# Optimization experiments

Measured on AMD Instinct MI355X. Metric: run time of the kernel, lower is better.

The kernel has to match this reference:

```python
import jax, jax.numpy as jnp
import numpy as np

N_NODES = 100000
N_EDGES = 1600000
IN_F = 16
HID = 128
N_LAYERS = 8
BN_EPS = 1e-5


def bn(x, gamma, beta):
    # BatchNorm1d in training mode: batch statistics over the node axis
    mu = jnp.mean(x, axis=0)
    var = jnp.var(x, axis=0)
    return gamma * (x - mu) * jax.lax.rsqrt(var + BN_EPS) + beta


def setup_inputs() -> dict:
    key = jax.random.key(0)
    ks = jax.random.split(key, 20)
    inp = {
        'x': jax.random.normal(ks[0], (N_NODES, IN_F), dtype=jnp.float32),
        'edge_index': jax.random.randint(ks[1], (2, N_EDGES), 0, N_NODES, dtype=jnp.int32),
        'eps': jnp.zeros((N_LAYERS,), jnp.float32),  # train_eps init 0
        # GIN MLPs: layer 0 has in_feature input, layers 1..7 have hidden input
        'W1_0': 0.1 * jax.random.normal(ks[2], (IN_F, HID), dtype=jnp.float32),
        'b1_0': jnp.zeros((HID,), jnp.float32),
        'W1': 0.1 * jax.random.normal(ks[3], (N_LAYERS - 1, HID, HID), dtype=jnp.float32),
        'b1': jnp.zeros((N_LAYERS - 1, HID), jnp.float32),
        'g_in': jnp.ones((N_LAYERS, HID), jnp.float32),   # inner MLP BatchNorm gamma
        'be_in': jnp.zeros((N_LAYERS, HID), jnp.float32),  # inner MLP BatchNorm beta
        'W2': 0.1 * jax.random.normal(ks[4], (N_LAYERS, HID, HID), dtype=jnp.float32),
        'b2': jnp.zeros((N_LAYERS, HID), jnp.float32),
        'g_out': jnp.ones((N_LAYERS, HID), jnp.float32),   # per-layer outer BatchNorm gamma
        'be_out': jnp.zeros((N_LAYERS, HID), jnp.float32),
        'Wr1': 0.1 * jax.random.normal(ks[5], (HID, HID), dtype=jnp.float32),
        'br1': jnp.zeros((HID,), jnp.float32),
        'gr': jnp.ones((HID,), jnp.float32),
        'ber': jnp.zeros((HID,), jnp.float32),
        'Wr2': 0.1 * jax.random.normal(ks[6], (HID, 1), dtype=jnp.float32),
        'br2': jnp.zeros((1,), jnp.float32),
    }
    return inp


def reference(x, edge_index, eps, W1_0, b1_0, W1, b1, g_in, be_in, W2, b2,
              g_out, be_out, Wr1, br1, gr, ber, Wr2, br2):
    src = edge_index[0]
    dst = edge_index[1]
    n = x.shape[0]
    h = x
    skip_sum = jnp.zeros((n, HID), x.dtype)
    for i in range(N_LAYERS):
        # GINConv: nn((1 + eps) * x + sum_{j in N(i)} x_j)
        agg = jax.ops.segment_sum(h[src], dst, num_segments=n)  # scatter-add over edges
        z = (1.0 + eps[i]) * h + agg
        Wa = W1_0 if i == 0 else W1[i - 1]
        ba = b1_0 if i == 0 else b1[i - 1]
        z = jax.nn.relu(bn(z @ Wa + ba, g_in[i], be_in[i]))  # MLP hidden layer (dropout=0)
        z = z @ W2[i] + b2[i]                                 # MLP output layer
        h = jax.nn.relu(bn(z, g_out[i], be_out[i]))           # outer BatchNorm + ReLU
        if i % 2 == 1:  # skips after layers 2, 4, 6, 8
            skip_sum = skip_sum + h
    h = skip_sum / 4.0
    r = jax.nn.relu(bn(h @ Wr1 + br1, gr, ber))
    return jax.nn.sigmoid(r @ Wr2 + br2)  # [N, 1]
```

## Files before the change

### kernel.cpp

```cpp
#include <hip/hip_runtime.h>
#include <hip/hip_bf16.h>

#define NNODES 100000
#define NEDGES 1600000
#define IN_F 16
#define HID 128
#define NLAYERS 8
#define BN_EPS 1e-5f
#define BLOBSZ 532480
#define NCLS 32

typedef __attribute__((ext_vector_type(8))) short short8;
typedef __attribute__((ext_vector_type(8))) _Float16 f16x8;
typedef __attribute__((ext_vector_type(4))) float f32x4;
typedef __attribute__((ext_vector_type(4))) unsigned int uint32x4;
typedef unsigned short ushort_t;
typedef unsigned int uint_t;

__device__ __forceinline__ float f16l(uint_t u) {
  return (float)__builtin_bit_cast(_Float16, (ushort_t)(u & 0xFFFFu));
}
__device__ __forceinline__ float f16h(uint_t u) {
  return (float)__builtin_bit_cast(_Float16, (ushort_t)(u >> 16));
}
// ... 20 lines not shown
__global__ __launch_bounds__(256) void bhist_kernel(
    const int* __restrict__ dst, int* __restrict__ bucketCnt, int E, int nbk) {
  __shared__ int cnt[256];
  int t = threadIdx.x;
  cnt[t] = 0;
  __syncthreads();
  int base = blockIdx.x * 2048 + t * 8;
#pragma unroll
  for (int j = 0; j < 8; ++j) {
    int i = base + j;
    if (i < E) atomicAdd(&cnt[dst[i] >> 9], 1);
  }
  __syncthreads();
  if (t < nbk && cnt[t]) atomicAdd(&bucketCnt[t], cnt[t]);
}

__global__ void bscan_kernel(const int* __restrict__ bucketCnt, int* __restrict__ bucketBase,
                             int* __restrict__ bucketCur, int* __restrict__ row_ptr,
                             int N, int E, int nbk) {
  __shared__ int s[256];
  int t = threadIdx.x;
  s[t] = (t < nbk) ? bucketCnt[t] : 0;
  __syncthreads();
  for (int off = 1; off < 256; off <<= 1) {
    int v = (t >= off) ? s[t - off] : 0;
    __syncthreads();
    s[t] += v;
    __syncthreads();
  }
  int excl = (t == 0) ? 0 : s[t - 1];
  if (t < nbk) { bucketBase[t] = excl; bucketCur[t] = excl; }
  if (t == nbk) bucketBase[t] = E;
  if (t == 0) row_ptr[N] = E;
}

__global__ __launch_bounds__(256) void bscatter_kernel(
    const int* __restrict__ src, const int* __restrict__ dst,
    int* __restrict__ bucketCur, int2* __restrict__ ebuf, int E, int nbk) {
  __shared__ int cnt[256];
  __shared__ int base_l[256];
  int t = threadIdx.x;
  cnt[t] = 0;
  __syncthreads();
  int base = blockIdx.x * 2048 + t * 8;
  int bj[8], lr[8], dj[8], sj[8];
#pragma unroll
  for (int j = 0; j < 8; ++j) {
    int i = base + j;
    if (i < E) {
      dj[j] = dst[i];
      sj[j] = src[i];
      bj[j] = dj[j] >> 9;
      lr[j] = atomicAdd(&cnt[bj[j]], 1);
    } else bj[j] = -1;
  }
  __syncthreads();
  if (t < nbk) base_l[t] = cnt[t] ? atomicAdd(&bucketCur[t], cnt[t]) : 0;
  __syncthreads();
#pragma unroll
  for (int j = 0; j < 8; ++j)
    if (bj[j] >= 0) ebuf[base_l[bj[j]] + lr[j]] = make_int2(dj[j], sj[j]);
}

__global__ __launch_bounds__(256) void bcsr_kernel(
    const int2* __restrict__ ebuf, const int* __restrict__ bucketBase,
    int* __restrict__ row_ptr, int* __restrict__ colb, int N) {
  __shared__ int h[512];
  __shared__ int cur[512];
  __shared__ int s2[256];
  int b = blockIdx.x, t = threadIdx.x;
  int beg = bucketBase[b], end = bucketBase[b + 1];
  h[t] = 0; h[t + 256] = 0;
  __syncthreads();
  for (int p = beg + t; p < end; p += 256) atomicAdd(&h[ebuf[p].x & 511], 1);
  __syncthreads();
  s2[t] = h[2 * t] + h[2 * t + 1];
  __syncthreads();
  for (int off = 1; off < 256; off <<= 1) {
    int v = (t >= off) ? s2[t - off] : 0;
    __syncthreads();
    s2[t] += v;
    __syncthreads();
  }
  int ep = (t == 0) ? 0 : s2[t - 1];
  cur[2 * t] = ep;
  cur[2 * t + 1] = ep + h[2 * t];
  int dg = (b << 9) + 2 * t;
  if (dg < N) row_ptr[dg] = beg + cur[2 * t];
  if (dg + 1 < N) row_ptr[dg + 1] = beg + cur[2 * t + 1];
  __syncthreads();
  for (int p = beg + t; p < end; p += 256) {
    int2 e2 = ebuf[p];
    int pos = beg + atomicAdd(&cur[e2.x & 511], 1);
    colb[pos] = e2.y;
  }
}

__global__ void preconv_kernel(const float* __restrict__ W1_0, const float* __restrict__ W1,
                               const float* __restrict__ W2, const float* __restrict__ Wr1,
                               ushort_t* __restrict__ WB) {
  int g = blockIdx.y;
  int e = blockIdx.x * 256 + threadIdx.x;
  int KP = (g == 0) ? 32 : 128;
  if (e >= KP * 128) return;
  int k = e >> 7, n = e & 127;
  float v;
  if (g == 0) v = (k < 16) ? W1_0[k * 128 + n] : 0.0f;
  else if (g <= 7) v = W1[(size_t)(g - 1) * 16384 + e];
  else if (g <= 15) v = W2[(size_t)(g - 8) * 16384 + e];
  else v = Wr1[e];
  size_t base = (g == 0) ? 0 : (8192 + (size_t)(g - 1) * 32768);
  int unit = ((k >> 5) << 9) + ((n >> 4) << 6) + (n & 15) + (((k >> 3) & 3) << 4);
  WB[base + (size_t)unit * 8 + (k & 7)] = __builtin_bit_cast(ushort_t, (_Float16)v);
}

__global__ __launch_bounds__(256) void agg16_kernel(
    const float* __restrict__ X, const int* __restrict__ rp, const int* __restrict__ colb,
    const float* __restrict__ eps, float* __restrict__ Z, int N) {
  int g = threadIdx.x >> 3;
  int l = threadIdx.x & 7;
  int n = blockIdx.x * 32 + g;
  if (n >= N) return;
  float e = 1.0f + eps[0];
  const float2* X2 = (const float2*)X;
  float2 self = X2[(size_t)n * 8 + l];
  float2 acc = make_float2(self.x * e, self.y * e);
  float2 acc2 = make_float2(0.0f, 0.0f);
  int beg = rp[n], end = rp[n + 1];
  int p = beg;
  for (; p + 4 <= end; p += 4) {
    int s0 = colb[p], s1 = colb[p + 1], s2 = colb[p + 2], s3 = colb[p + 3];
    float2 v0 = X2[(size_t)s0 * 8 + l];
    float2 v1 = X2[(size_t)s1 * 8 + l];
    float2 v2 = X2[(size_t)s2 * 8 + l];
    float2 v3 = X2[(size_t)s3 * 8 + l];
    acc.x += v0.x; acc.y += v0.y;
    acc2.x += v1.x; acc2.y += v1.y;
    acc.x += v2.x; acc.y += v2.y;
    acc2.x += v3.x; acc2.y += v3.y;
  }
  for (; p < end; ++p) {
    int s = colb[p];
    float2 v = X2[(size_t)s * 8 + l];
    acc.x += v.x; acc.y += v.y;
  }
  acc.x += acc2.x; acc.y += acc2.y;
  ((float2*)Z)[(size_t)n * 8 + l] = acc;
}

__global__ __launch_bounds__(256) void agg128_kernel(
    const ushort_t* __restrict__ Y, const float* __restrict__ av, const float* __restrict__ cv,
    const int* __restrict__ rp, const int* __restrict__ colb,
    const float* __restrict__ eps, int layer, uint_t* __restrict__ Z,
    float* __restrict__ SKIP, int smode, int N) {
  int wv = threadIdx.x >> 6;
  int lane = threadIdx.x & 63;
  int half = lane >> 5;
  int l32 = lane & 31;
  int n = blockIdx.x * 4 + wv;
  if (n >= N) return;
  float e = 1.0f + eps[layer];
  float4 a4 = *(const float4*)(av + l32 * 4);
  float4 c4 = *(const float4*)(cv + l32 * 4);
  const uint2* Y2 = (const uint2*)Y;
  uint2 sv = Y2[(size_t)n * 32 + l32];
  float h0 = fmaxf(fmaf(a4.x, f16l(sv.x), c4.x), 0.0f);
  float h1 = fmaxf(fmaf(a4.y, f16h(sv.x), c4.y), 0.0f);
  float h2 = fmaxf(fmaf(a4.z, f16l(sv.y), c4.z), 0.0f);
  float h3 = fmaxf(fmaf(a4.w, f16h(sv.y), c4.w), 0.0f);
  if (half == 0) {
    if (smode == 1) {
      ((float4*)SKIP)[(size_t)n * 32 + l32] = make_float4(h0, h1, h2, h3);
    } else if (smode == 2) {
      float4* S4 = (float4*)SKIP;
      float4 s = S4[(size_t)n * 32 + l32];
      s.x += h0; s.y += h1; s.z += h2; s.w += h3;
      S4[(size_t)n * 32 + l32] = s;
    }
  }
  float ax0 = half ? 0.0f : h0 * e;
  float ax1 = half ? 0.0f : h1 * e;
  float ax2 = half ? 0.0f : h2 * e;
  float ax3 = half ? 0.0f : h3 * e;
  float bx0 = 0.0f, bx1 = 0.0f, bx2 = 0.0f, bx3 = 0.0f;
  int beg = rp[n], end = rp[n + 1];
  int p = beg;
  for (; p + 8 <= end; p += 8) {
    int s0 = colb[p + half];
    int s1 = colb[p + 2 + half];
    int s2 = colb[p + 4 + half];
    int s3 = colb[p + 6 + half];
    uint2 v0 = Y2[(size_t)s0 * 32 + l32];
    uint2 v1 = Y2[(size_t)s1 * 32 + l32];
    uint2 v2 = Y2[(size_t)s2 * 32 + l32];
    uint2 v3 = Y2[(size_t)s3 * 32 + l32];
    ax0 += fmaxf(fmaf(a4.x, f16l(v0.x), c4.x), 0.0f);
    ax1 += fmaxf(fmaf(a4.y, f16h(v0.x), c4.y), 0.0f);
    ax2 += fmaxf(fmaf(a4.z, f16l(v0.y), c4.z), 0.0f);
    ax3 += fmaxf(fmaf(a4.w, f16h(v0.y), c4.w), 0.0f);
    bx0 += fmaxf(fmaf(a4.x, f16l(v1.x), c4.x), 0.0f);
    bx1 += fmaxf(fmaf(a4.y, f16h(v1.x), c4.y), 0.0f);
    bx2 += fmaxf(fmaf(a4.z, f16l(v1.y), c4.z), 0.0f);
    bx3 += fmaxf(fmaf(a4.w, f16h(v1.y), c4.w), 0.0f);
    ax0 += fmaxf(fmaf(a4.x, f16l(v2.x), c4.x), 0.0f);
    ax1 += fmaxf(fmaf(a4.y, f16h(v2.x), c4.y), 0.0f);
    ax2 += fmaxf(fmaf(a4.z, f16l(v2.y), c4.z), 0.0f);
    ax3 += fmaxf(fmaf(a4.w, f16h(v2.y), c4.w), 0.0f);
    bx0 += fmaxf(fmaf(a4.x, f16l(v3.x), c4.x), 0.0f);
    bx1 += fmaxf(fmaf(a4.y, f16h(v3.x), c4.y), 0.0f);
    bx2 += fmaxf(fmaf(a4.z, f16l(v3.y), c4.z), 0.0f);
    bx3 += fmaxf(fmaf(a4.w, f16h(v3.y), c4.w), 0.0f);
  }
  for (; p + 2 <= end; p += 2) {
    int s = colb[p + half];
    uint2 v = Y2[(size_t)s * 32 + l32];
    ax0 += fmaxf(fmaf(a4.x, f16l(v.x), c4.x), 0.0f);
    ax1 += fmaxf(fmaf(a4.y, f16h(v.x), c4.y), 0.0f);
    ax2 += fmaxf(fmaf(a4.z, f16l(v.y), c4.z), 0.0f);
    ax3 += fmaxf(fmaf(a4.w, f16h(v.y), c4.w), 0.0f);
  }
  if (p < end && half == 0) {
    int s = colb[p];
    uint2 v = Y2[(size_t)s * 32 + l32];
    ax0 += fmaxf(fmaf(a4.x, f16l(v.x), c4.x), 0.0f);
    ax1 += fmaxf(fmaf(a4.y, f16h(v.x), c4.y), 0.0f);
    ax2 += fmaxf(fmaf(a4.z, f16l(v.y), c4.z), 0.0f);
    ax3 += fmaxf(fmaf(a4.w, f16h(v.y), c4.w), 0.0f);
  }
  ax0 += bx0; ax1 += bx1; ax2 += bx2; ax3 += bx3;
  ax0 += __shfl_xor(ax0, 32, 64);
  ax1 += __shfl_xor(ax1, 32, 64);
  ax2 += __shfl_xor(ax2, 32, 64);
  ax3 += __shfl_xor(ax3, 32, 64);
  if (half == 0) {
    uint2 o;
    o.x = pk16(ax0, ax1);
    o.y = pk16(ax2, ax3);
    ((uint2*)Z)[(size_t)n * 32 + l32] = o;
  }
}

template <int KTOT, int MODE, int OUT>
__global__ __launch_bounds__(256, 4) void gemm_mfma(
    const float* __restrict__ A, const ushort_t* __restrict__ A2u,
    const ushort_t* __restrict__ Bhi,
    const float* __restrict__ bias,
    const float* __restrict__ pa, const float* __restrict__ pc,
    void* __restrict__ Cv,
    float* __restrict__ gstat,
    float* __restrict__ aout, float* __restrict__ cout, int* __restrict__ cnt,
    const float* __restrict__ gamma, const float* __restrict__ beta,
    float invN, int M, int nb) {
  __shared__ float s_part[4][256];
  __shared__ int s_last;
  const int tid = threadIdx.x;
  const int w = tid >> 6;
  const int lane = tid & 63;
  const int ln = lane & 15;
  const int quad = lane >> 4;
  const int brow = blockIdx.x * 128;
  constexpr int AST = (MODE == 3) ? 16 : 128;

  int r0 = brow + (w << 5) + ln;       if (r0 >= M) r0 = M - 1;
  int r1 = brow + (w << 5) + 16 + ln;  if (r1 >= M) r1 = M - 1;

  f32x4 acc[2][8];
#pragma unroll
  for (int rt = 0; rt < 2; ++rt)
#pragma unroll
    for (int ct = 0; ct < 8; ++ct) acc[rt][ct] = (f32x4){0.0f, 0.0f, 0.0f, 0.0f};

  constexpr int KC = KTOT / 32;
#pragma unroll
  for (int kcl = 0; kcl < KC; ++kcl) {
    const int kb = (kcl << 5) + (quad << 3);
    f16x8 af0, af1;
    if constexpr (MODE == 0) {
      af0 = __builtin_bit_cast(f16x8, ntl_s8(A2u + (size_t)r0 * 128 + kb));
      af1 = __builtin_bit_cast(f16x8, ntl_s8(A2u + (size_t)r1 * 128 + kb));
    } else if constexpr (MODE == 1) {
      uint32x4 xa = *(const uint32x4*)(A2u + (size_t)r0 * 128 + kb);
      uint32x4 xb = *(const uint32x4*)(A2u + (size_t)r1 * 128 + kb);
      float4 p0 = *(const float4*)(pa + kb);
      float4 p1 = *(const float4*)(pa + kb + 4);
      float4 q0 = *(const float4*)(pc + kb);
      float4 q1 = *(const float4*)(pc + kb + 4);
      float pp[8] = {p0.x, p0.y, p0.z, p0.w, p1.x, p1.y, p1.z, p1.w};
      float qq[8] = {q0.x, q0.y, q0.z, q0.w, q1.x, q1.y, q1.z, q1.w};
      float e0[8] = {f16l(xa.x), f16h(xa.x), f16l(xa.y), f16h(xa.y),
                     f16l(xa.z), f16h(xa.z), f16l(xa.w), f16h(xa.w)};
      float e1[8] = {f16l(xb.x), f16h(xb.x), f16l(xb.y), f16h(xb.y),
                     f16l(xb.z), f16h(xb.z), f16l(xb.w), f16h(xb.w)};
#pragma unroll
      for (int j = 0; j < 8; ++j) {
        e0[j] = fmaxf(fmaf(pp[j], e0[j], qq[j]), 0.0f);
        e1[j] = fmaxf(fmaf(pp[j], e1[j], qq[j]), 0.0f);
      }
      af0 = pack8(e0);
      af1 = pack8(e1);
    } else if constexpr (MODE == 2) {
      f32x4 a0 = ntl4(A + (size_t)r0 * AST + kb);
      f32x4 a1 = ntl4(A + (size_t)r0 * AST + kb + 4);
      f32x4 b0 = ntl4(A + (size_t)r1 * AST + kb);
      f32x4 b1 = ntl4(A + (size_t)r1 * AST + kb + 4);
      float s0[8] = {a0.x, a0.y, a0.z, a0.w, a1.x, a1.y, a1.z, a1.w};
      float s1[8] = {b0.x, b0.y, b0.z, b0.w, b1.x, b1.y, b1.z, b1.w};
      uint32x4 ya = *(const uint32x4*)(A2u + (size_t)r0 * 128 + kb);
      uint32x4 yb = *(const uint32x4*)(A2u + (size_t)r1 * 128 + kb);
      float4 p0 = *(const float4*)(pa + kb);
      float4 p1 = *(const float4*)(pa + kb + 4);
      float4 q0 = *(const float4*)(pc + kb);
      float4 q1 = *(const float4*)(pc + kb + 4);
      float pp[8] = {p0.x, p0.y, p0.z, p0.w, p1.x, p1.y, p1.z, p1.w};
      float qq[8] = {q0.x, q0.y, q0.z, q0.w, q1.x, q1.y, q1.z, q1.w};
      float y0a[8] = {f16l(ya.x), f16h(ya.x), f16l(ya.y), f16h(ya.y),
                      f16l(ya.z), f16h(ya.z), f16l(ya.w), f16h(ya.w)};
      float y1a[8] = {f16l(yb.x), f16h(yb.x), f16l(yb.y), f16h(yb.y),
                      f16l(yb.z), f16h(yb.z), f16l(yb.w), f16h(yb.w)};
      float e0[8], e1[8];
#pragma unroll
      for (int j = 0; j < 8; ++j) {
        e0[j] = 0.25f * (s0[j] + fmaxf(fmaf(pp[j], y0a[j], qq[j]), 0.0f));
        e1[j] = 0.25f * (s1[j] + fmaxf(fmaf(pp[j], y1a[j], qq[j]), 0.0f));
      }
      af0 = pack8(e0);
      af1 = pack8(e1);
    } else {
      if (kb < 16) {
        f32x4 a0 = ntl4(A + (size_t)r0 * AST + kb);
        f32x4 a1 = ntl4(A + (size_t)r0 * AST + kb + 4);
        f32x4 b0 = ntl4(A + (size_t)r1 * AST + kb);
        f32x4 b1 = ntl4(A + (size_t)r1 * AST + kb + 4);
        float e0[8] = {a0.x, a0.y, a0.z, a0.w, a1.x, a1.y, a1.z, a1.w};
        float e1[8] = {b0.x, b0.y, b0.z, b0.w, b1.x, b1.y, b1.z, b1.w};
        af0 = pack8(e0);
        af1 = pack8(e1);
      } else {
#pragma unroll
        for (int j = 0; j < 8; ++j) { af0[j] = (_Float16)0.0f; af1[j] = (_Float16)0.0f; }
      }
    }
    const ushort_t* bh_base = Bhi + (((size_t)(kcl << 9) + lane) << 3);
#pragma unroll
    for (int ct = 0; ct < 8; ++ct) {
      f16x8 bh = __builtin_bit_cast(f16x8, *(const short8*)(bh_base + (ct << 9)));
      acc[0][ct] = __builtin_amdgcn_mfma_f32_16x16x32_f16(af0, bh, acc[0][ct], 0, 0, 0);
      acc[1][ct] = __builtin_amdgcn_mfma_f32_16x16x32_f16(af1, bh, acc[1][ct], 0, 0, 0);
    }
  }

#pragma unroll
  for (int ct = 0; ct < 8; ++ct) {
    int col = (ct << 4) + ln;
    float bsc = bias[col];
    float csum = 0.0f, csq = 0.0f;
#pragma unroll
    for (int rt = 0; rt < 2; ++rt) {
#pragma unroll
      for (int i = 0; i < 4; ++i) {
        int row = brow + (w << 5) + (rt << 4) + (quad << 2) + i;
        if (row < M) {
          float y = acc[rt][ct][i] + bsc;
          csum += y; csq += y * y;
          if constexpr (OUT == 0) {
            ((float*)Cv)[(size_t)row * 128 + col] = y;
          } else {
            ((ushort_t*)Cv)[(size_t)row * 128 + col] = f2h(y);
          }
        }
      }
    }
    csum += __shfl_xor(csum, 16, 64);
    csum += __shfl_xor(csum, 32, 64);
    csq += __shfl_xor(csq, 16, 64);
    csq += __shfl_xor(csq, 32, 64);
    if (quad == 0) {
      s_part[w][col] = csum;
      s_part[w][128 + col] = csq;
    }
  }
  __syncthreads();
  const int cls = (int)(blockIdx.x & (NCLS - 1));
  {
    float v = s_part[0][tid] + s_part[1][tid] + s_part[2][tid] + s_part[3][tid];
    atomicAdd(&gstat[(cls << 8) + tid], v);
  }
  __syncthreads();
  if (tid == 0) {
    s_last = 0;
    int clsCnt = (nb >> 5) + ((cls < (nb & (NCLS - 1))) ? 1 : 0);
    int v = __hip_atomic_fetch_add(&cnt[cls], 1, __ATOMIC_RELAXED, __HIP_MEMORY_SCOPE_AGENT);
    if (v == clsCnt - 1) {
      int vm = __hip_atomic_fetch_add(&cnt[NCLS], 1, __ATOMIC_RELAXED, __HIP_MEMORY_SCOPE_AGENT);
      if (vm == NCLS - 1) s_last = 1;
    }
  }
  __syncthreads();
  if (s_last && tid < 128) {
    float s = 0.0f, q = 0.0f;
#pragma unroll
    for (int c = 0; c < NCLS; ++c) {
      s += __hip_atomic_load(&gstat[(c << 8) + tid], __ATOMIC_RELAXED, __HIP_MEMORY_SCOPE_AGENT);
      q += __hip_atomic_load(&gstat[(c << 8) + 128 + tid], __ATOMIC_RELAXED,
                             __HIP_MEMORY_SCOPE_AGENT);
    }
    float mu = s * invN;
    float var = q * invN - mu * mu;
    float sc = gamma[tid] * rsqrtf(var + BN_EPS);
    aout[tid] = sc;
    cout[tid] = beta[tid] - sc * mu;
  }
}

__global__ __launch_bounds__(256) void finaldot_kernel(
    const ushort_t* __restrict__ Y, const float* __restrict__ a, const float* __restrict__ c,
    const float* __restrict__ Wr2, const float* __restrict__ br2,
    float* __restrict__ out, int N) {
  int wv = threadIdx.x >> 6;
  int lane = threadIdx.x & 63;
  int n = blockIdx.x * 4 + wv;
  if (n >= N) return;
  uint_t yv = ((const uint_t*)Y)[(size_t)n * 64 + lane];
  int c0 = lane * 2;
  float s = fmaxf(fmaf(a[c0], f16l(yv), c[c0]), 0.0f) * Wr2[c0] +
            fmaxf(fmaf(a[c0 + 1], f16h(yv), c[c0 + 1]), 0.0f) * Wr2[c0 + 1];
  for (int off = 32; off > 0; off >>= 1) s += __shfl_down(s, off, 64);
  if (lane == 0) out[n] = 1.0f / (1.0f + expf(-(s + br2[0])));
}

extern "C" void kernel_launch(void* const* d_in, const int* in_sizes, int n_in,
                              void* d_out, int out_size, void* d_ws, size_t ws_size,
                              hipStream_t stream) {
  const float* x     = (const float*)d_in[0];
  const int*   ei    = (const int*)d_in[1];
  const float* eps   = (const float*)d_in[2];
  const float* W1_0  = (const float*)d_in[3];
  const float* b1_0  = (const float*)d_in[4];
  const float* W1    = (const float*)d_in[5];
  const float* b1    = (const float*)d_in[6];
  const float* g_in  = (const float*)d_in[7];
  const float* be_in = (const float*)d_in[8];
  const float* W2    = (const float*)d_in[9];
  const float* b2    = (const float*)d_in[10];
  const float* g_out = (const float*)d_in[11];
  const float* be_out= (const float*)d_in[12];
  const float* Wr1   = (const float*)d_in[13];
  const float* br1   = (const float*)d_in[14];
  const float* gr    = (const float*)d_in[15];
  const float* ber   = (const float*)d_in[16];
  const float* Wr2   = (const float*)d_in[17];
  const float* br2   = (const float*)d_in[18];
  float* out = (float*)d_out;

  const int N = in_sizes[0] / IN_F;
  const int E = in_sizes[1] / 2;
  const int* srcv = ei;
  const int* dstv = ei + E;
  const int nbk = (N + 511) >> 9;

  float* X0    = (float*)d_ws;
  float* SKIP  = X0 + (size_t)N * HID;
  ushort_t* YB = (ushort_t*)(SKIP + (size_t)N * HID);
  int* colb    = (int*)(YB + (size_t)N * HID);
  int* row_ptr = colb + E;
  int2* ebuf   = (int2*)(row_ptr + (N + 4));
  int* bucketCnt  = (int*)(ebuf + E);
  int* bucketBase = bucketCnt + 256;
  int* bucketCur  = bucketBase + 260;
  float* arena = (float*)(bucketCur + 256);
  ushort_t* WB = (ushort_t*)(arena + 17 * 8512);
  ushort_t* X0u = (ushort_t*)X0;

  hipMemsetAsync(bucketCnt, 0, sizeof(int) * 256, stream);
  hipMemsetAsync(arena, 0, sizeof(float) * 17 * 8512, stream);

  int nbE = (E + 2047) / 2048;
  bhist_kernel<<<nbE, 256, 0, stream>>>(dstv, bucketCnt, E, nbk);
  bscan_kernel<<<1, 256, 0, stream>>>(bucketCnt, bucketBase, bucketCur, row_ptr, N, E, nbk);
  bscatter_kernel<<<nbE, 256, 0, stream>>>(srcv, dstv, bucketCur, ebuf, E, nbk);
  bcsr_kernel<<<nbk, 256, 0, stream>>>(ebuf, bucketBase, row_ptr, colb, N);
  preconv_kernel<<<dim3(64, 17), 256, 0, stream>>>(W1_0, W1, W2, Wr1, WB);

  const int gg = (N + 127) / 128;
  const float invN = 1.0f / (float)N;
#define SLOT(s) (arena + (s) * 8512)
#define SSTAT(s) SLOT(s)
#define SA(s)   (SLOT(s) + 8192)
#define SC(s)   (SLOT(s) + 8320)
#define SCNT(s) ((int*)(SLOT(s) + 8448))
#define WBH(g)  (WB + ((g) == 0 ? 0 : (8192 + (size_t)((g) - 1) * 32768)))

  agg16_kernel<<<(N + 31) / 32, 256, 0, stream>>>(x, row_ptr, colb, eps, SKIP, N);
  gemm_mfma<32, 3, 1><<<gg, 256, 0, stream>>>(
      SKIP, nullptr, WBH(0), b1_0, nullptr, nullptr, X0u,
      SSTAT(0), SA(0), SC(0), SCNT(0), g_in, be_in, invN, N, gg);
  gemm_mfma<128, 1, 1><<<gg, 256, 0, stream>>>(
      nullptr, X0u, WBH(8), b2, SA(0), SC(0), YB,
      SSTAT(1), SA(1), SC(1), SCNT(1), g_out, be_out, invN, N, gg);

  for (int L = 1; L < NLAYERS; ++L) {
    int sp = 2 * L - 1;
    int s0 = 2 * L, s1 = 2 * L + 1;
    int smode = ((L - 1) & 1) ? ((L == 2) ? 1 : 2) : 0;
    agg128_kernel<<<(N + 3) / 4, 256, 0, stream>>>(
        YB, SA(sp), SC(sp), row_ptr, colb, eps, L, (uint_t*)X0u, SKIP, smode, N);
    gemm_mfma<128, 0, 1><<<gg, 256, 0, stream>>>(
        nullptr, X0u, WBH(L), b1 + (size_t)(L - 1) * HID, nullptr, nullptr, X0u,
        SSTAT(s0), SA(s0), SC(s0), SCNT(s0),
        g_in + (size_t)L * HID, be_in + (size_t)L * HID, invN, N, gg);
    gemm_mfma<128, 1, 1><<<gg, 256, 0, stream>>>(
        nullptr, X0u, WBH(8 + L), b2 + (size_t)L * HID, SA(s0), SC(s0), YB,
        SSTAT(s1), SA(s1), SC(s1), SCNT(s1),
        g_out + (size_t)L * HID, be_out + (size_t)L * HID, invN, N, gg);
  }

  gemm_mfma<128, 2, 1><<<gg, 256, 0, stream>>>(
      SKIP, YB, WBH(16), br1, SA(15), SC(15), X0u,
      SSTAT(16), SA(16), SC(16), SCNT(16), gr, ber, invN, N, gg);
  finaldot_kernel<<<(N + 3) / 4, 256, 0, stream>>>(X0u, SA(16), SC(16), Wr2, br2, out, N);
#undef SLOT
#undef SSTAT
#undef SA
#undef SC
#undef SCNT
#undef WBH
}
```

Measured before the change: 1.180 ms.

## Fuse each layer's two MLP GEMMs into one kernel with grid-wide BN barrier

Adds a gemm_pair kernel that runs the first MLP GEMM, keeps its fp16 output tile in shared memory, and computes the inner BatchNorm statistics across the grid. Blocks then spin on a global flag set by the last-arriving block before applying BN+ReLU and running the second GEMM from LDS. This removes one kernel launch per layer and the global write and re-read of the hidden activation. The cost is larger LDS use per block and a grid-wide spin barrier, which deadlocks unless all blocks are co-resident on the GPU. The old gemm_mfma is reduced to the one mode still in use.

```diff
diff --git a/kernel.cpp b/kernel.cpp
--- a/kernel.cpp
+++ b/kernel.cpp
@@ -284,6 +284,235 @@
   }
 }
 
+template <int MODE1>
+__global__ __launch_bounds__(256, 4) void gemm_pair(
+    const float* __restrict__ A, const ushort_t* __restrict__ A2u,
+    const ushort_t* __restrict__ Bh1, const float* __restrict__ bias1,
+    const ushort_t* __restrict__ Bh2, const float* __restrict__ bias2,
+    ushort_t* __restrict__ YB,
+    float* __restrict__ gstat1, int* __restrict__ cnt1, int* __restrict__ flag1,
+    float* __restrict__ pa1, float* __restrict__ pc1,
+    const float* __restrict__ g1, const float* __restrict__ be1,
+    float* __restrict__ gstat2, float* __restrict__ aout2, float* __restrict__ cout2,
+    int* __restrict__ cnt2,
+    const float* __restrict__ g2, const float* __restrict__ be2,
+    float invN, int M, int nb) {
+  __shared__ ushort_t h1s[128][136];
+  __shared__ float s_part[4][256];
+  __shared__ float s_papc[256];
+  __shared__ int s_last;
+  const int tid = threadIdx.x;
+  const int w = tid >> 6;
+  const int lane = tid & 63;
+  const int ln = lane & 15;
+  const int quad = lane >> 4;
+  const int brow = blockIdx.x * 128;
+  const int cls = (int)(blockIdx.x & (NCLS - 1));
+
+  int r0 = brow + (w << 5) + ln;       if (r0 >= M) r0 = M - 1;
+  int r1 = brow + (w << 5) + 16 + ln;  if (r1 >= M) r1 = M - 1;
+
+  f32x4 acc[2][8];
+#pragma unroll
+  for (int rt = 0; rt < 2; ++rt)
+#pragma unroll
+    for (int ct = 0; ct < 8; ++ct) acc[rt][ct] = (f32x4){0.0f, 0.0f, 0.0f, 0.0f};
+
+  constexpr int KC1 = (MODE1 == 3) ? 1 : 4;
+#pragma unroll
+  for (int kcl = 0; kcl < KC1; ++kcl) {
+    const int kb = (kcl << 5) + (quad << 3);
+    f16x8 af0, af1;
+    if constexpr (MODE1 == 3) {
+      if (kb < 16) {
+        f32x4 a0 = ntl4(A + (size_t)r0 * 16 + kb);
+        f32x4 a1 = ntl4(A + (size_t)r0 * 16 + kb + 4);
+        f32x4 b0 = ntl4(A + (size_t)r1 * 16 + kb);
+        f32x4 b1 = ntl4(A + (size_t)r1 * 16 + kb + 4);
+        float e0[8] = {a0.x, a0.y, a0.z, a0.w, a1.x, a1.y, a1.z, a1.w};
+        float e1[8] = {b0.x, b0.y, b0.z, b0.w, b1.x, b1.y, b1.z, b1.w};
+        af0 = pack8(e0);
+        af1 = pack8(e1);
+      } else {
+#pragma unroll
+        for (int j = 0; j < 8; ++j) { af0[j] = (_Float16)0.0f; af1[j] = (_Float16)0.0f; }
+      }
+    } else {
+      af0 = __builtin_bit_cast(f16x8, ntl_s8(A2u + (size_t)r0 * 128 + kb));
+      af1 = __builtin_bit_cast(f16x8, ntl_s8(A2u + (size_t)r1 * 128 + kb));
+    }
+    const ushort_t* bh_base = Bh1 + (((size_t)(kcl << 9) + lane) << 3);
+#pragma unroll
+    for (int ct = 0; ct < 8; ++ct) {
+      f16x8 bh = __builtin_bit_cast(f16x8, *(const short8*)(bh_base + (ct << 9)));
+      acc[0][ct] = __builtin_amdgcn_mfma_f32_16x16x32_f16(af0, bh, acc[0][ct], 0, 0, 0);
+      acc[1][ct] = __builtin_amdgcn_mfma_f32_16x16x32_f16(af1, bh, acc[1][ct], 0, 0, 0);
+    }
+  }
+
+#pragma unroll
+  for (int ct = 0; ct < 8; ++ct) {
+    int col = (ct << 4) + ln;
+    float bsc = bias1[col];
+    float csum = 0.0f, csq = 0.0f;
+#pragma unroll
+    for (int rt = 0; rt < 2; ++rt) {
+#pragma unroll
+      for (int i = 0; i < 4; ++i) {
+        int rl = (w << 5) + (rt << 4) + (quad << 2) + i;
+        float y = acc[rt][ct][i] + bsc;
+        h1s[rl][col] = f2h(y);
+        if (brow + rl < M) { csum += y; csq += y * y; }
+      }
+    }
+    csum += __shfl_xor(csum, 16, 64);
+    csum += __shfl_xor(csum, 32, 64);
+    csq += __shfl_xor(csq, 16, 64);
+    csq += __shfl_xor(csq, 32, 64);
+    if (quad == 0) {
+      s_part[w][col] = csum;
+      s_part[w][128 + col] = csq;
+    }
+  }
+  __syncthreads();
+  {
+    float v = s_part[0][tid] + s_part[1][tid] + s_part[2][tid] + s_part[3][tid];
+    atomicAdd(&gstat1[(cls << 8) + tid], v);
+  }
+  __syncthreads();
+  if (tid == 0) {
+    s_last = 0;
+    int clsCnt = (nb >> 5) + ((cls < (nb & (NCLS - 1))) ? 1 : 0);
+    int v = __hip_atomic_fetch_add(&cnt1[cls], 1, __ATOMIC_RELAXED, __HIP_MEMORY_SCOPE_AGENT);
+    if (v == clsCnt - 1) {
+      int vm = __hip_atomic_fetch_add(&cnt1[NCLS], 1, __ATOMIC_RELAXED, __HIP_MEMORY_SCOPE_AGENT);
+      if (vm == NCLS - 1) s_last = 1;
+    }
+  }
+  __syncthreads();
+  if (s_last && tid < 128) {
+    float s = 0.0f, q = 0.0f;
+#pragma unroll
+    for (int c = 0; c < NCLS; ++c) {
+      s += __hip_atomic_load(&gstat1[(c << 8) + tid], __ATOMIC_RELAXED, __HIP_MEMORY_SCOPE_AGENT);
+      q += __hip_atomic_load(&gstat1[(c << 8) + 128 + tid], __ATOMIC_RELAXED,
+                             __HIP_MEMORY_SCOPE_AGENT);
+    }
+    float mu = s * invN;
+    float var = q * invN - mu * mu;
+    float sc = g1[tid] * rsqrtf(var + BN_EPS);
+    __hip_atomic_store(&pa1[tid], sc, __ATOMIC_RELAXED, __HIP_MEMORY_SCOPE_AGENT);
+    __hip_atomic_store(&pc1[tid], be1[tid] - sc * mu, __ATOMIC_RELAXED,
+                       __HIP_MEMORY_SCOPE_AGENT);
+  }
+  __syncthreads();
+  if (s_last && tid == 0)
+    __hip_atomic_store(flag1, 1, __ATOMIC_RELEASE, __HIP_MEMORY_SCOPE_AGENT);
+  if (tid == 0) {
+    while (__hip_atomic_load(flag1, __ATOMIC_RELAXED, __HIP_MEMORY_SCOPE_AGENT) == 0)
+      __builtin_amdgcn_s_sleep(8);
+    (void)__hip_atomic_load(flag1, __ATOMIC_ACQUIRE, __HIP_MEMORY_SCOPE_AGENT);
+  }
+  __syncthreads();
+  s_papc[tid] = (tid < 128)
+      ? __hip_atomic_load(&pa1[tid], __ATOMIC_RELAXED, __HIP_MEMORY_SCOPE_AGENT)
+      : __hip_atomic_load(&pc1[tid - 128], __ATOMIC_RELAXED, __HIP_MEMORY_SCOPE_AGENT);
+  __syncthreads();
+
+#pragma unroll
+  for (int rt = 0; rt < 2; ++rt)
+#pragma unroll
+    for (int ct = 0; ct < 8; ++ct) acc[rt][ct] = (f32x4){0.0f, 0.0f, 0.0f, 0.0f};
+
+#pragma unroll
+  for (int kcl = 0; kcl < 4; ++kcl) {
+    const int kb = (kcl << 5) + (quad << 3);
+    uint32x4 xa = *(const uint32x4*)&h1s[(w << 5) + ln][kb];
+    uint32x4 xb = *(const uint32x4*)&h1s[(w << 5) + 16 + ln][kb];
+    float pp[8], qq[8];
+#pragma unroll
+    for (int j = 0; j < 8; ++j) {
+      pp[j] = s_papc[kb + j];
+      qq[j] = s_papc[128 + kb + j];
+    }
+    float e0[8] = {f16l(xa.x), f16h(xa.x), f16l(xa.y), f16h(xa.y),
+                   f16l(xa.z), f16h(xa.z), f16l(xa.w), f16h(xa.w)};
+    float e1[8] = {f16l(xb.x), f16h(xb.x), f16l(xb.y), f16h(xb.y),
+                   f16l(xb.z), f16h(xb.z), f16l(xb.w), f16h(xb.w)};
+#pragma unroll
+    for (int j = 0; j < 8; ++j) {
+      e0[j] = fmaxf(fmaf(pp[j], e0[j], qq[j]), 0.0f);
+      e1[j] = fmaxf(fmaf(pp[j], e1[j], qq[j]), 0.0f);
+    }
+    f16x8 af0 = pack8(e0);
+    f16x8 af1 = pack8(e1);
+    const ushort_t* bh_base = Bh2 + (((size_t)(kcl << 9) + lane) << 3);
+#pragma unroll
+    for (int ct = 0; ct < 8; ++ct) {
+      f16x8 bh = __builtin_bit_cast(f16x8, *(const short8*)(bh_base + (ct << 9)));
+      acc[0][ct] = __builtin_amdgcn_mfma_f32_16x16x32_f16(af0, bh, acc[0][ct], 0, 0, 0);
+      acc[1][ct] = __builtin_amdgcn_mfma_f32_16x16x32_f16(af1, bh, acc[1][ct], 0, 0, 0);
+    }
+  }
+
+#pragma unroll
+  for (int ct = 0; ct < 8; ++ct) {
+    int col = (ct << 4) + ln;
+    float bsc = bias2[col];
+    float csum = 0.0f, csq = 0.0f;
+#pragma unroll
+    for (int rt = 0; rt < 2; ++rt) {
+#pragma unroll
+      for (int i = 0; i < 4; ++i) {
+        int row = brow + (w << 5) + (rt << 4) + (quad << 2) + i;
+        if (row < M) {
+          float y = acc[rt][ct][i] + bsc;
+          csum += y; csq += y * y;
+          YB[(size_t)row * 128 + col] = f2h(y);
+        }
+      }
+    }
+    csum += __shfl_xor(csum, 16, 64);
+    csum += __shfl_xor(csum, 32, 64);
+    csq += __shfl_xor(csq, 16, 64);
+    csq += __shfl_xor(csq, 32, 64);
+    if (quad == 0) {
+      s_part[w][col] = csum;
+      s_part[w][128 + col] = csq;
+    }
+  }
+  __syncthreads();
+  {
+    float v = s_part[0][tid] + s_part[1][tid] + s_part[2][tid] + s_part[3][tid];
+    atomicAdd(&gstat2[(cls << 8) + tid], v);
+  }
+  __syncthreads();
+  if (tid == 0) {
+    s_last = 0;
+    int clsCnt = (nb >> 5) + ((cls < (nb & (NCLS - 1))) ? 1 : 0);
+    int v = __hip_atomic_fetch_add(&cnt2[cls], 1, __ATOMIC_RELAXED, __HIP_MEMORY_SCOPE_AGENT);
+    if (v == clsCnt - 1) {
+      int vm = __hip_atomic_fetch_add(&cnt2[NCLS], 1, __ATOMIC_RELAXED, __HIP_MEMORY_SCOPE_AGENT);
+      if (vm == NCLS - 1) s_last = 1;
+    }
+  }
+  __syncthreads();
+  if (s_last && tid < 128) {
+    float s = 0.0f, q = 0.0f;
+#pragma unroll
+    for (int c = 0; c < NCLS; ++c) {
+      s += __hip_atomic_load(&gstat2[(c << 8) + tid], __ATOMIC_RELAXED, __HIP_MEMORY_SCOPE_AGENT);
+      q += __hip_atomic_load(&gstat2[(c << 8) + 128 + tid], __ATOMIC_RELAXED,
+                             __HIP_MEMORY_SCOPE_AGENT);
+    }
+    float mu = s * invN;
+    float var = q * invN - mu * mu;
+    float sc = g2[tid] * rsqrtf(var + BN_EPS);
+    aout2[tid] = sc;
+    cout2[tid] = be2[tid] - sc * mu;
+  }
+}
+
 template <int KTOT, int MODE, int OUT>
 __global__ __launch_bounds__(256, 4) void gemm_mfma(
     const float* __restrict__ A, const ushort_t* __restrict__ A2u,
@@ -303,7 +532,7 @@
   const int ln = lane & 15;
   const int quad = lane >> 4;
   const int brow = blockIdx.x * 128;
-  constexpr int AST = (MODE == 3) ? 16 : 128;
+  constexpr int AST = 128;
 
   int r0 = brow + (w << 5) + ln;       if (r0 >= M) r0 = M - 1;
   int r1 = brow + (w << 5) + 16 + ln;  if (r1 >= M) r1 = M - 1;
@@ -318,72 +547,32 @@
 #pragma unroll
   for (int kcl = 0; kcl < KC; ++kcl) {
     const int kb = (kcl << 5) + (quad << 3);
-    f16x8 af0, af1;
-    if constexpr (MODE == 0) {
-      af0 = __builtin_bit_cast(f16x8, ntl_s8(A2u + (size_t)r0 * 128 + kb));
-      af1 = __builtin_bit_cast(f16x8, ntl_s8(A2u + (size_t)r1 * 128 + kb));
-    } else if constexpr (MODE == 1) {
-      uint32x4 xa = *(const uint32x4*)(A2u + (size_t)r0 * 128 + kb);
-      uint32x4 xb = *(const uint32x4*)(A2u + (size_t)r1 * 128 + kb);
-      float4 p0 = *(const float4*)(pa + kb);
-      float4 p1 = *(const float4*)(pa + kb + 4);
-      float4 q0 = *(const float4*)(pc + kb);
-      float4 q1 = *(const float4*)(pc + kb + 4);
-      float pp[8] = {p0.x, p0.y, p0.z, p0.w, p1.x, p1.y, p1.z, p1.w};
-      float qq[8] = {q0.x, q0.y, q0.z, q0.w, q1.x, q1.y, q1.z, q1.w};
-      float e0[8] = {f16l(xa.x), f16h(xa.x), f16l(xa.y), f16h(xa.y),
-                     f16l(xa.z), f16h(xa.z), f16l(xa.w), f16h(xa.w)};
-      float e1[8] = {f16l(xb.x), f16h(xb.x), f16l(xb.y), f16h(xb.y),
-                     f16l(xb.z), f16h(xb.z), f16l(xb.w), f16h(xb.w)};
-#pragma unroll
-      for (int j = 0; j < 8; ++j) {
-        e0[j] = fmaxf(fmaf(pp[j], e0[j], qq[j]), 0.0f);
-        e1[j] = fmaxf(fmaf(pp[j], e1[j], qq[j]), 0.0f);
-      }
-      af0 = pack8(e0);
-      af1 = pack8(e1);
-    } else if constexpr (MODE == 2) {
-      f32x4 a0 = ntl4(A + (size_t)r0 * AST + kb);
-      f32x4 a1 = ntl4(A + (size_t)r0 * AST + kb + 4);
-      f32x4 b0 = ntl4(A + (size_t)r1 * AST + kb);
-      f32x4 b1 = ntl4(A + (size_t)r1 * AST + kb + 4);
-      float s0[8] = {a0.x, a0.y, a0.z, a0.w, a1.x, a1.y, a1.z, a1.w};
-      float s1[8] = {b0.x, b0.y, b0.z, b0.w, b1.x, b1.y, b1.z, b1.w};
-      uint32x4 ya = *(const uint32x4*)(A2u + (size_t)r0 * 128 + kb);
-      uint32x4 yb = *(const uint32x4*)(A2u + (size_t)r1 * 128 + kb);
-      float4 p0 = *(const float4*)(pa + kb);
-      float4 p1 = *(const float4*)(pa + kb + 4);
-      float4 q0 = *(const float4*)(pc + kb);
-      float4 q1 = *(const float4*)(pc + kb + 4);
-      float pp[8] = {p0.x, p0.y, p0.z, p0.w, p1.x, p1.y, p1.z, p1.w};
-      float qq[8] = {q0.x, q0.y, q0.z, q0.w, q1.x, q1.y, q1.z, q1.w};
-      float y0a[8] = {f16l(ya.x), f16h(ya.x), f16l(ya.y), f16h(ya.y),
-                      f16l(ya.z), f16h(ya.z), f16l(ya.w), f16h(ya.w)};
-      float y1a[8] = {f16l(yb.x), f16h(yb.x), f16l(yb.y), f16h(yb.y),
-                      f16l(yb.z), f16h(yb.z), f16l(yb.w), f16h(yb.w)};
-      float e0[8], e1[8];
-#pragma unroll
-      for (int j = 0; j < 8; ++j) {
-        e0[j] = 0.25f * (s0[j] + fmaxf(fmaf(pp[j], y0a[j], qq[j]), 0.0f));
-        e1[j] = 0.25f * (s1[j] + fmaxf(fmaf(pp[j], y1a[j], qq[j]), 0.0f));
-      }
-      af0 = pack8(e0);
-      af1 = pack8(e1);
-    } else {
-      if (kb < 16) {
-        f32x4 a0 = ntl4(A + (size_t)r0 * AST + kb);
-        f32x4 a1 = ntl4(A + (size_t)r0 * AST + kb + 4);
-        f32x4 b0 = ntl4(A + (size_t)r1 * AST + kb);
-        f32x4 b1 = ntl4(A + (size_t)r1 * AST + kb + 4);
-        float e0[8] = {a0.x, a0.y, a0.z, a0.w, a1.x, a1.y, a1.z, a1.w};
-        float e1[8] = {b0.x, b0.y, b0.z, b0.w, b1.x, b1.y, b1.z, b1.w};
-        af0 = pack8(e0);
-        af1 = pack8(e1);
-      } else {
-#pragma unroll
-        for (int j = 0; j < 8; ++j) { af0[j] = (_Float16)0.0f; af1[j] = (_Float16)0.0f; }
-      }
-    }
+    f32x4 a0 = ntl4(A + (size_t)r0 * AST + kb);
+    f32x4 a1 = ntl4(A + (size_t)r0 * AST + kb + 4);
+    f32x4 b0 = ntl4(A + (size_t)r1 * AST + kb);
+    f32x4 b1 = ntl4(A + (size_t)r1 * AST + kb + 4);
+    float s0[8] = {a0.x, a0.y, a0.z, a0.w, a1.x, a1.y, a1.z, a1.w};
+    float s1[8] = {b0.x, b0.y, b0.z, b0.w, b1.x, b1.y, b1.z, b1.w};
+    uint32x4 ya = *(const uint32x4*)(A2u + (size_t)r0 * 128 + kb);
+    uint32x4 yb = *(const uint32x4*)(A2u + (size_t)r1 * 128 + kb);
+    float4 p0 = *(const float4*)(pa + kb);
+    float4 p1 = *(const float4*)(pa + kb + 4);
+    float4 q0 = *(const float4*)(pc + kb);
+    float4 q1 = *(const float4*)(pc + kb + 4);
+    float pp[8] = {p0.x, p0.y, p0.z, p0.w, p1.x, p1.y, p1.z, p1.w};
+    float qq[8] = {q0.x, q0.y, q0.z, q0.w, q1.x, q1.y, q1.z, q1.w};
+    float y0a[8] = {f16l(ya.x), f16h(ya.x), f16l(ya.y), f16h(ya.y),
+                    f16l(ya.z), f16h(ya.z), f16l(ya.w), f16h(ya.w)};
+    float y1a[8] = {f16l(yb.x), f16h(yb.x), f16l(yb.y), f16h(yb.y),
+                    f16l(yb.z), f16h(yb.z), f16l(yb.w), f16h(yb.w)};
+    float e0[8], e1[8];
+#pragma unroll
+    for (int j = 0; j < 8; ++j) {
+      e0[j] = 0.25f * (s0[j] + fmaxf(fmaf(pp[j], y0a[j], qq[j]), 0.0f));
+      e1[j] = 0.25f * (s1[j] + fmaxf(fmaf(pp[j], y1a[j], qq[j]), 0.0f));
+    }
+    f16x8 af0 = pack8(e0);
+    f16x8 af1 = pack8(e1);
     const ushort_t* bh_base = Bhi + (((size_t)(kcl << 9) + lane) << 3);
 #pragma unroll
     for (int ct = 0; ct < 8; ++ct) {
@@ -406,11 +595,7 @@
         if (row < M) {
           float y = acc[rt][ct][i] + bsc;
           csum += y; csq += y * y;
-          if constexpr (OUT == 0) {
-            ((float*)Cv)[(size_t)row * 128 + col] = y;
-          } else {
-            ((ushort_t*)Cv)[(size_t)row * 128 + col] = f2h(y);
-          }
+          ((ushort_t*)Cv)[(size_t)row * 128 + col] = f2h(y);
         }
       }
     }
@@ -532,14 +717,13 @@
 #define SA(s)   (SLOT(s) + 8192)
 #define SC(s)   (SLOT(s) + 8320)
 #define SCNT(s) ((int*)(SLOT(s) + 8448))
+#define SFLG(s) ((int*)(SLOT(s) + 8481))
 #define WBH(g)  (WB + ((g) == 0 ? 0 : (8192 + (size_t)((g) - 1) * 32768)))
 
   agg16_kernel<<<(N + 31) / 32, 256, 0, stream>>>(x, row_ptr, colb, eps, SKIP, N);
-  gemm_mfma<32, 3, 1><<<gg, 256, 0, stream>>>(
-      SKIP, nullptr, WBH(0), b1_0, nullptr, nullptr, X0u,
-      SSTAT(0), SA(0), SC(0), SCNT(0), g_in, be_in, invN, N, gg);
-  gemm_mfma<128, 1, 1><<<gg, 256, 0, stream>>>(
-      nullptr, X0u, WBH(8), b2, SA(0), SC(0), YB,
+  gemm_pair<3><<<gg, 256, 0, stream>>>(
+      SKIP, nullptr, WBH(0), b1_0, WBH(8), b2, YB,
+      SSTAT(0), SCNT(0), SFLG(0), SA(0), SC(0), g_in, be_in,
       SSTAT(1), SA(1), SC(1), SCNT(1), g_out, be_out, invN, N, gg);
 
   for (int L = 1; L < NLAYERS; ++L) {
@@ -548,12 +732,10 @@
     int smode = ((L - 1) & 1) ? ((L == 2) ? 1 : 2) : 0;
     agg128_kernel<<<(N + 3) / 4, 256, 0, stream>>>(
         YB, SA(sp), SC(sp), row_ptr, colb, eps, L, (uint_t*)X0u, SKIP, smode, N);
-    gemm_mfma<128, 0, 1><<<gg, 256, 0, stream>>>(
-        nullptr, X0u, WBH(L), b1 + (size_t)(L - 1) * HID, nullptr, nullptr, X0u,
-        SSTAT(s0), SA(s0), SC(s0), SCNT(s0),
-        g_in + (size_t)L * HID, be_in + (size_t)L * HID, invN, N, gg);
-    gemm_mfma<128, 1, 1><<<gg, 256, 0, stream>>>(
-        nullptr, X0u, WBH(8 + L), b2 + (size_t)L * HID, SA(s0), SC(s0), YB,
+    gemm_pair<0><<<gg, 256, 0, stream>>>(
+        nullptr, X0u, WBH(L), b1 + (size_t)(L - 1) * HID, WBH(8 + L), b2 + (size_t)L * HID, YB,
+        SSTAT(s0), SCNT(s0), SFLG(s0), SA(s0), SC(s0),
+        g_in + (size_t)L * HID, be_in + (size_t)L * HID,
         SSTAT(s1), SA(s1), SC(s1), SCNT(s1),
         g_out + (size_t)L * HID, be_out + (size_t)L * HID, invN, N, gg);
   }
@@ -567,5 +749,6 @@
 #undef SA
 #undef SC
 #undef SCNT
+#undef SFLG
 #undef WBH
 }
```

Result: slower. 1.213 ms (+2.8%).

## Store skip accumulator in fp16 and widen aggregation gathers to 16-byte loads

Applied to the files above, without the earlier changes.

The skip-sum buffer changes from fp32 to packed fp16. This halves its read-modify-write traffic in the aggregation kernel and its reads in the regressor GEMM. The 128-wide aggregation kernel now has 16 lanes each load 8 halves (16 bytes) per neighbor row, with four edges handled per wave step instead of two, and two xor shuffles reduce the partials. Accumulating the skip sum in fp16 loses precision, and wave lanes sit idle more often on nodes with few neighbors.

```diff
diff --git a/kernel.cpp b/kernel.cpp
--- a/kernel.cpp
+++ b/kernel.cpp
@@ -196,91 +196,102 @@
     const ushort_t* __restrict__ Y, const float* __restrict__ av, const float* __restrict__ cv,
     const int* __restrict__ rp, const int* __restrict__ colb,
     const float* __restrict__ eps, int layer, uint_t* __restrict__ Z,
-    float* __restrict__ SKIP, int smode, int N) {
+    ushort_t* __restrict__ SKIP, int smode, int N) {
   int wv = threadIdx.x >> 6;
   int lane = threadIdx.x & 63;
-  int half = lane >> 5;
-  int l32 = lane & 31;
+  int quad = lane >> 4;
+  int l16 = lane & 15;
   int n = blockIdx.x * 4 + wv;
   if (n >= N) return;
   float e = 1.0f + eps[layer];
-  float4 a4 = *(const float4*)(av + l32 * 4);
-  float4 c4 = *(const float4*)(cv + l32 * 4);
-  const uint2* Y2 = (const uint2*)Y;
-  uint2 sv = Y2[(size_t)n * 32 + l32];
-  float h0 = fmaxf(fmaf(a4.x, f16l(sv.x), c4.x), 0.0f);
-  float h1 = fmaxf(fmaf(a4.y, f16h(sv.x), c4.y), 0.0f);
-  float h2 = fmaxf(fmaf(a4.z, f16l(sv.y), c4.z), 0.0f);
-  float h3 = fmaxf(fmaf(a4.w, f16h(sv.y), c4.w), 0.0f);
-  if (half == 0) {
+  float4 aA = *(const float4*)(av + l16 * 8);
+  float4 aB = *(const float4*)(av + l16 * 8 + 4);
+  float4 cA = *(const float4*)(cv + l16 * 8);
+  float4 cB = *(const float4*)(cv + l16 * 8 + 4);
+  float a8[8] = {aA.x, aA.y, aA.z, aA.w, aB.x, aB.y, aB.z, aB.w};
+  float c8[8] = {cA.x, cA.y, cA.z, cA.w, cB.x, cB.y, cB.z, cB.w};
+  const uint32x4* Y4 = (const uint32x4*)Y;
+
+  uint32x4 sv = Y4[(size_t)n * 16 + l16];
+  uint_t svp[4] = {sv.x, sv.y, sv.z, sv.w};
+  float h[8];
+#pragma unroll
+  for (int j = 0; j < 4; ++j) {
+    h[2 * j]     = fmaxf(fmaf(a8[2 * j],     f16l(svp[j]), c8[2 * j]), 0.0f);
+    h[2 * j + 1] = fmaxf(fmaf(a8[2 * j + 1], f16h(svp[j]), c8[2 * j + 1]), 0.0f);
+  }
+  if (quad == 0) {
     if (smode == 1) {
-      ((float4*)SKIP)[(size_t)n * 32 + l32] = make_float4(h0, h1, h2, h3);
+      uint32x4 o = {pk16(h[0], h[1]), pk16(h[2], h[3]), pk16(h[4], h[5]), pk16(h[6], h[7])};
+      ((uint32x4*)SKIP)[(size_t)n * 16 + l16] = o;
     } else if (smode == 2) {
-      float4* S4 = (float4*)SKIP;
-      float4 s = S4[(size_t)n * 32 + l32];
-      s.x += h0; s.y += h1; s.z += h2; s.w += h3;
-      S4[(size_t)n * 32 + l32] = s;
-    }
-  }
-  float ax0 = half ? 0.0f : h0 * e;
-  float ax1 = half ? 0.0f : h1 * e;
-  float ax2 = half ? 0.0f : h2 * e;
-  float ax3 = half ? 0.0f : h3 * e;
-  float bx0 = 0.0f, bx1 = 0.0f, bx2 = 0.0f, bx3 = 0.0f;
+      uint32x4 s = ((const uint32x4*)SKIP)[(size_t)n * 16 + l16];
+      uint_t sp[4] = {s.x, s.y, s.z, s.w};
+      uint_t op[4];
+#pragma unroll
+      for (int j = 0; j < 4; ++j)
+        op[j] = pk16(f16l(sp[j]) + h[2 * j], f16h(sp[j]) + h[2 * j + 1]);
+      uint32x4 o = {op[0], op[1], op[2], op[3]};
+      ((uint32x4*)SKIP)[(size_t)n * 16 + l16] = o;
+    }
+  }
+  float acc[8], acc2[8];
+#pragma unroll
+  for (int j = 0; j < 8; ++j) {
+    acc[j] = (quad == 0) ? h[j] * e : 0.0f;
+    acc2[j] = 0.0f;
+  }
   int beg = rp[n], end = rp[n + 1];
   int p = beg;
   for (; p + 8 <= end; p += 8) {
-    int s0 = colb[p + half];
-    int s1 = colb[p + 2 + half];
-    int s2 = colb[p + 4 + half];
-    int s3 = colb[p + 6 + half];
-    uint2 v0 = Y2[(size_t)s0 * 32 + l32];
-    uint2 v1 = Y2[(size_t)s1 * 32 + l32];
-    uint2 v2 = Y2[(size_t)s2 * 32 + l32];
-    uint2 v3 = Y2[(size_t)s3 * 32 + l32];
-    ax0 += fmaxf(fmaf(a4.x, f16l(v0.x), c4.x), 0.0f);
-    ax1 += fmaxf(fmaf(a4.y, f16h(v0.x), c4.y), 0.0f);
-    ax2 += fmaxf(fmaf(a4.z, f16l(v0.y), c4.z), 0.0f);
-    ax3 += fmaxf(fmaf(a4.w, f16h(v0.y), c4.w), 0.0f);
-    bx0 += fmaxf(fmaf(a4.x, f16l(v1.x), c4.x), 0.0f);
-    bx1 += fmaxf(fmaf(a4.y, f16h(v1.x), c4.y), 0.0f);
-    bx2 += fmaxf(fmaf(a4.z, f16l(v1.y), c4.z), 0.0f);
-    bx3 += fmaxf(fmaf(a4.w, f16h(v1.y), c4.w), 0.0f);
-    ax0 += fmaxf(fmaf(a4.x, f16l(v2.x), c4.x), 0.0f);
-    ax1 += fmaxf(fmaf(a4.y, f16h(v2.x), c4.y), 0.0f);
-    ax2 += fmaxf(fmaf(a4.z, f16l(v2.y), c4.z), 0.0f);
-    ax3 += fmaxf(fmaf(a4.w, f16h(v2.y), c4.w), 0.0f);
-    bx0 += fmaxf(fmaf(a4.x, f16l(v3.x), c4.x), 0.0f);
-    bx1 += fmaxf(fmaf(a4.y, f16h(v3.x), c4.y), 0.0f);
-    bx2 += fmaxf(fmaf(a4.z, f16l(v3.y), c4.z), 0.0f);
-    bx3 += fmaxf(fmaf(a4.w, f16h(v3.y), c4.w), 0.0f);
-  }
-  for (; p + 2 <= end; p += 2) {
-    int s = colb[p + half];
-    uint2 v = Y2[(size_t)s * 32 + l32];
-    ax0 += fmaxf(fmaf(a4.x, f16l(v.x), c4.x), 0.0f);
-    ax1 += fmaxf(fmaf(a4.y, f16h(v.x), c4.y), 0.0f);
-    ax2 += fmaxf(fmaf(a4.z, f16l(v.y), c4.z), 0.0f);
-    ax3 += fmaxf(fmaf(a4.w, f16h(v.y), c4.w), 0.0f);
-  }
-  if (p < end && half == 0) {
-    int s = colb[p];
-    uint2 v = Y2[(size_t)s * 32 + l32];
-    ax0 += fmaxf(fmaf(a4.x, f16l(v.x), c4.x), 0.0f);
-    ax1 += fmaxf(fmaf(a4.y, f16h(v.x), c4.y), 0.0f);
-    ax2 += fmaxf(fmaf(a4.z, f16l(v.y), c4.z), 0.0f);
-    ax3 += fmaxf(fmaf(a4.w, f16h(v.y), c4.w), 0.0f);
-  }
-  ax0 += bx0; ax1 += bx1; ax2 += bx2; ax3 += bx3;
-  ax0 += __shfl_xor(ax0, 32, 64);
-  ax1 += __shfl_xor(ax1, 32, 64);
-  ax2 += __shfl_xor(ax2, 32, 64);
-  ax3 += __shfl_xor(ax3, 32, 64);
-  if (half == 0) {
-    uint2 o;
-    o.x = pk16(ax0, ax1);
-    o.y = pk16(ax2, ax3);
-    ((uint2*)Z)[(size_t)n * 32 + l32] = o;
+    int s0 = colb[p + quad];
+    int s1 = colb[p + 4 + quad];
+    uint32x4 v0 = Y4[(size_t)s0 * 16 + l16];
+    uint32x4 v1 = Y4[(size_t)s1 * 16 + l16];
+    uint_t v0p[4] = {v0.x, v0.y, v0.z, v0.w};
+    uint_t v1p[4] = {v1.x, v1.y, v1.z, v1.w};
+#pragma unroll
+    for (int j = 0; j < 4; ++j) {
+      acc[2 * j]      += fmaxf(fmaf(a8[2 * j],     f16l(v0p[j]), c8[2 * j]), 0.0f);
+      acc[2 * j + 1]  += fmaxf(fmaf(a8[2 * j + 1], f16h(v0p[j]), c8[2 * j + 1]), 0.0f);
+      acc2[2 * j]     += fmaxf(fmaf(a8[2 * j],     f16l(v1p[j]), c8[2 * j]), 0.0f);
+      acc2[2 * j + 1] += fmaxf(fmaf(a8[2 * j + 1], f16h(v1p[j]), c8[2 * j + 1]), 0.0f);
+    }
+  }
+  if (p + 4 <= end) {
+    int s = colb[p + quad];
+    uint32x4 v = Y4[(size_t)s * 16 + l16];
+    uint_t vp[4] = {v.x, v.y, v.z, v.w};
+#pragma unroll
+    for (int j = 0; j < 4; ++j) {
+      acc[2 * j]     += fmaxf(fmaf(a8[2 * j],     f16l(vp[j]), c8[2 * j]), 0.0f);
+      acc[2 * j + 1] += fmaxf(fmaf(a8[2 * j + 1], f16h(vp[j]), c8[2 * j + 1]), 0.0f);
+    }
+    p += 4;
+  }
+  if (p + quad < end) {
+    int s = colb[p + quad];
+    uint32x4 v = Y4[(size_t)s * 16 + l16];
+    uint_t vp[4] = {v.x, v.y, v.z, v.w};
+#pragma unroll
+    for (int j = 0; j < 4; ++j) {
+      acc2[2 * j]     += fmaxf(fmaf(a8[2 * j],     f16l(vp[j]), c8[2 * j]), 0.0f);
+      acc2[2 * j + 1] += fmaxf(fmaf(a8[2 * j + 1], f16h(vp[j]), c8[2 * j + 1]), 0.0f);
+    }
+  }
+  uint_t op[4];
+#pragma unroll
+  for (int j = 0; j < 8; ++j) {
+    float t = acc[j] + acc2[j];
+    t += __shfl_xor(t, 16, 64);
+    t += __shfl_xor(t, 32, 64);
+    acc[j] = t;
+  }
+  if (quad == 0) {
+#pragma unroll
+    for (int j = 0; j < 4; ++j) op[j] = pk16(acc[2 * j], acc[2 * j + 1]);
+    uint32x4 o = {op[0], op[1], op[2], op[3]};
+    ((uint32x4*)Z)[(size_t)n * 16 + l16] = o;
   }
 }
 
@@ -303,7 +314,6 @@
   const int ln = lane & 15;
   const int quad = lane >> 4;
   const int brow = blockIdx.x * 128;
-  constexpr int AST = (MODE == 3) ? 16 : 128;
 
   int r0 = brow + (w << 5) + ln;       if (r0 >= M) r0 = M - 1;
   int r1 = brow + (w << 5) + 16 + ln;  if (r1 >= M) r1 = M - 1;
@@ -343,12 +353,13 @@
       af0 = pack8(e0);
       af1 = pack8(e1);
     } else if constexpr (MODE == 2) {
-      f32x4 a0 = ntl4(A + (size_t)r0 * AST + kb);
-      f32x4 a1 = ntl4(A + (size_t)r0 * AST + kb + 4);
-      f32x4 b0 = ntl4(A + (size_t)r1 * AST + kb);
-      f32x4 b1 = ntl4(A + (size_t)r1 * AST + kb + 4);
-      float s0[8] = {a0.x, a0.y, a0.z, a0.w, a1.x, a1.y, a1.z, a1.w};
-      float s1[8] = {b0.x, b0.y, b0.z, b0.w, b1.x, b1.y, b1.z, b1.w};
+      const ushort_t* Au = (const ushort_t*)A;
+      uint32x4 sa = *(const uint32x4*)(Au + (size_t)r0 * 128 + kb);
+      uint32x4 sb = *(const uint32x4*)(Au + (size_t)r1 * 128 + kb);
+      float s0[8] = {f16l(sa.x), f16h(sa.x), f16l(sa.y), f16h(sa.y),
+                     f16l(sa.z), f16h(sa.z), f16l(sa.w), f16h(sa.w)};
+      float s1[8] = {f16l(sb.x), f16h(sb.x), f16l(sb.y), f16h(sb.y),
+                     f16l(sb.z), f16h(sb.z), f16l(sb.w), f16h(sb.w)};
       uint32x4 ya = *(const uint32x4*)(A2u + (size_t)r0 * 128 + kb);
       uint32x4 yb = *(const uint32x4*)(A2u + (size_t)r1 * 128 + kb);
       float4 p0 = *(const float4*)(pa + kb);
@@ -371,10 +382,10 @@
       af1 = pack8(e1);
     } else {
       if (kb < 16) {
-        f32x4 a0 = ntl4(A + (size_t)r0 * AST + kb);
-        f32x4 a1 = ntl4(A + (size_t)r0 * AST + kb + 4);
-        f32x4 b0 = ntl4(A + (size_t)r1 * AST + kb);
-        f32x4 b1 = ntl4(A + (size_t)r1 * AST + kb + 4);
+        f32x4 a0 = ntl4(A + (size_t)r0 * 16 + kb);
+        f32x4 a1 = ntl4(A + (size_t)r0 * 16 + kb + 4);
+        f32x4 b0 = ntl4(A + (size_t)r1 * 16 + kb);
+        f32x4 b1 = ntl4(A + (size_t)r1 * 16 + kb + 4);
         float e0[8] = {a0.x, a0.y, a0.z, a0.w, a1.x, a1.y, a1.z, a1.w};
         float e1[8] = {b0.x, b0.y, b0.z, b0.w, b1.x, b1.y, b1.z, b1.w};
         af0 = pack8(e0);
@@ -514,6 +525,7 @@
   float* arena = (float*)(bucketCur + 256);
   ushort_t* WB = (ushort_t*)(arena + 17 * 8512);
   ushort_t* X0u = (ushort_t*)X0;
+  ushort_t* SKIPu = (ushort_t*)SKIP;
 
   hipMemsetAsync(bucketCnt, 0, sizeof(int) * 256, stream);
   hipMemsetAsync(arena, 0, sizeof(float) * 17 * 8512, stream);
@@ -547,7 +559,7 @@
     int s0 = 2 * L, s1 = 2 * L + 1;
     int smode = ((L - 1) & 1) ? ((L == 2) ? 1 : 2) : 0;
     agg128_kernel<<<(N + 3) / 4, 256, 0, stream>>>(
-        YB, SA(sp), SC(sp), row_ptr, colb, eps, L, (uint_t*)X0u, SKIP, smode, N);
+        YB, SA(sp), SC(sp), row_ptr, colb, eps, L, (uint_t*)X0u, SKIPu, smode, N);
     gemm_mfma<128, 0, 1><<<gg, 256, 0, stream>>>(
         nullptr, X0u, WBH(L), b1 + (size_t)(L - 1) * HID, nullptr, nullptr, X0u,
         SSTAT(s0), SA(s0), SC(s0), SCNT(s0),
@@ -559,7 +571,7 @@
   }
 
   gemm_mfma<128, 2, 1><<<gg, 256, 0, stream>>>(
-      SKIP, YB, WBH(16), br1, SA(15), SC(15), X0u,
+      (const float*)SKIPu, YB, WBH(16), br1, SA(15), SC(15), X0u,
       SSTAT(16), SA(16), SC(16), SCNT(16), gr, ber, invN, N, gg);
   finaldot_kernel<<<(N + 3) / 4, 256, 0, stream>>>(X0u, SA(16), SC(16), Wr2, br2, out, N);
 #undef SLOT
```

Result: faster. 1.133 ms (-4.0%).
